# Kernel optimization log

Measured on AMD Instinct MI355X. Metric: run time of the kernel, lower is better.

The kernel has to match this reference:

```python
import jax, jax.numpy as jnp
import numpy as np

CLIP_TANH = 10.0
M_CHECKS, N_VARS = 256, 512   # parity-check matrix shape
ROW_W = 8                     # ones per check row -> E = 256*8 = 2048 edges
BATCH = 16384


def _build_masks():
    """Tanner-graph connectivity masks, as in init_w_skipconn2even / initialize_w_v2c."""
    rng = np.random.default_rng(0)
    pcm = np.zeros((M_CHECKS, N_VARS), np.float32)
    for r in range(M_CHECKS):
        pcm[r, rng.choice(N_VARS, ROW_W, replace=False)] = 1.0
    checks, variables = np.nonzero(pcm)  # edge list, row-major order, length E
    E = checks.size
    # edge e' feeds edge e iff same variable node, different check node
    same_var = variables[:, None] == variables[None, :]
    diff_chk = checks[:, None] != checks[None, :]
    w_odd2even_mask = (same_var & diff_chk).astype(np.float32)               # [E, E]
    # variable v feeds every edge incident to it
    w_skip_mask = (np.arange(N_VARS)[:, None] == variables[None, :]).astype(np.float32)  # [N, E]
    return jnp.asarray(w_odd2even_mask), jnp.asarray(w_skip_mask), E


def setup_inputs() -> dict:
    key = jax.random.key(0)
    w_o2e_mask, w_skip_mask, E = _build_masks()
    k = jax.random.split(key, 5)
    return {
        "x": jax.random.normal(k[0], (BATCH, E), jnp.float32),          # edge messages
        "llr": jax.random.normal(k[1], (BATCH, N_VARS), jnp.float32),   # channel LLRs
        "u": jax.random.uniform(k[2], (E,), jnp.float32),               # dropout uniforms
        "odd_weights": 0.05 * jax.random.normal(k[3], (E, E), jnp.float32),
        "llr_weights": 1.0 + 0.05 * jax.random.normal(k[4], (N_VARS, E), jnp.float32),
        "dropout_logits": 10.0 * jnp.ones((E,), jnp.float32),           # 10000*LOGITS_INIT analogue (sigmoid ~ 1)
        "w_odd2even_mask": w_o2e_mask,
        "w_skipconn2even_mask": w_skip_mask,
    }


def reference(x, llr, u, odd_weights, llr_weights, dropout_logits,
              w_odd2even_mask, w_skipconn2even_mask):
    # TEST-phase forward, mask_only=False
    total_mask = w_odd2even_mask * odd_weights                        # [E, E], very sparse support
    z = (u < jax.nn.sigmoid(dropout_logits)).astype(x.dtype)          # Bernoulli gate per source edge
    mask_after_dropout = total_mask * z[:, None]                      # row-wise gating
    msg = x @ mask_after_dropout                                      # [B, E]
    skip = llr @ (w_skipconn2even_mask * llr_weights)                 # [B, E]
    odd_clamp = jnp.clip(msg + skip, -CLIP_TANH, CLIP_TANH)
    return jnp.tanh(0.5 * odd_clamp)
```

## Files before the change

### kernel.cpp

```cpp
#include <hip/hip_runtime.h>
#include <hip/hip_bf16.h>

constexpr int E     = 2048;
constexpr int NVARS = 512;
constexpr int DMAX  = 20;
constexpr int TB    = 8;
constexpr int NT    = 512;

__device__ __forceinline__ unsigned bf16hi(float f) {
    const unsigned uu = __float_as_uint(f);
    return (uu + 0x7FFFu + ((uu >> 16) & 1u)) & 0xFFFF0000u;
}
__device__ __forceinline__ unsigned pk2(float a, float b) {
    return (bf16hi(a) >> 16) | bf16hi(b);
}
__device__ __forceinline__ float bl(unsigned q) { return __uint_as_float(q << 16); }
__device__ __forceinline__ float bh(unsigned q) { return __uint_as_float(q & 0xFFFF0000u); }

__global__ __launch_bounds__(256)
void k_vsrc(const float* __restrict__ skip_mask,
            const float* __restrict__ llr_w,
            unsigned short* __restrict__ vsrc,
            float* __restrict__ skw)
{
    const int col = blockIdx.x * 256 + threadIdx.x;
    const int v0  = blockIdx.y * (NVARS / 32);
    for (int v = v0; v < v0 + NVARS / 32; ++v) {
        const float m = skip_mask[(size_t)v * E + col];
        if (m != 0.0f) {
            vsrc[col] = (unsigned short)v;
            skw [col] = m * llr_w[(size_t)v * E + col];
        }
    }
}

__global__ __launch_bounds__(64)
void k_pervar(const unsigned short* __restrict__ vsrc,
              const float* __restrict__ skw,
              const float* __restrict__ odd_w,
              const float* __restrict__ u,
              const float* __restrict__ logits,
              unsigned short* __restrict__ mcol,
              unsigned short* __restrict__ wt,
              unsigned int*   __restrict__ itemMeta,
              int*            __restrict__ nitems,
              float2*         __restrict__ meta)
{
    __shared__ unsigned short vs[E];
    __shared__ int deg[NVARS];
    __shared__ unsigned short mem[DMAX];
    __shared__ float zf[DMAX];

    const int v   = blockIdx.x;
    const int tid = threadIdx.x;

    for (int i = tid; i < E / 8; i += 64)
        ((uint4*)vs)[i] = ((const uint4*)vsrc)[i];
    for (int i = tid; i < NVARS; i += 64) deg[i] = 0;
    __syncthreads();
    for (int i = tid; i < E; i += 64) atomicAdd(&deg[vs[i]], 1);
    __syncthreads();

    const int dv = deg[v];

    int itot = 0, vst = 0, ib = 0;
    for (int i = tid; i < NVARS; i += 64) {
        const int d2 = deg[i];
        if (!d2) continue;
        const int dc = (d2 < DMAX) ? d2 : DMAX;
        const int ic = (dc + 3) >> 2;
        itot += ic;
        if (dv > 0 && (d2 < dv || (d2 == dv && i < v))) { vst += d2; ib += ic; }
    }
    #pragma unroll
    for (int o = 32; o; o >>= 1) {
        itot += __shfl_xor(itot, o);
        vst  += __shfl_xor(vst,  o);
        ib   += __shfl_xor(ib,   o);
    }
    if (v == 0 && tid == 0) nitems[0] = itot;
    if (!dv) return;
    const int de = (dv < DMAX) ? dv : DMAX;

    int cnt = 0;
    for (int c = 0; c < E / 64; ++c) {
        const int e = c * 64 + tid;
        const bool m = ((int)vs[e] == v);
        const unsigned long long bal = __ballot(m);
        if (m) {
            const int pos = cnt + __popcll(bal & ((1ull << tid) - 1ull));
            if (pos < DMAX) mem[pos] = (unsigned short)e;
        }
        cnt += __popcll(bal);
    }
    __syncthreads();

    if (tid < de) {
        const int m = mem[tid];
        const float sig = 1.0f / (1.0f + __expf(-logits[m]));
        zf[tid] = (u[m] < sig) ? 1.0f : 0.0f;
        mcol[vst + tid] = (unsigned short)m;
        meta[vst + tid] = make_float2(skw[m], __int_as_float(m | (v << 11)));
    }
    __syncthreads();

    for (int idx = tid; idx < de * de; idx += 64) {
        const int j = idx / de;
        const int i = idx - j * de;
        float ww = 0.0f;
        if (i != j)
            ww = odd_w[(size_t)mem[j] * E + mem[i]] * zf[j];
        wt[(size_t)(vst + j) * DMAX + i] = (unsigned short)(bf16hi(ww) >> 16);
    }

    const int nch = (de + 3) >> 2;
    if (tid < nch)
        itemMeta[ib + tid] = (unsigned)vst | ((unsigned)tid << 11)
                           | ((unsigned)de << 14);
}

__device__ __forceinline__ float th(float s) {
    float c = fminf(fmaxf(s, -10.0f), 10.0f);
    float t = __expf(c);
    return (t - 1.0f) * __frcp_rn(t + 1.0f);
}

__global__ __launch_bounds__(NT, 4)
void fused_main(const float* __restrict__ x,
                const float* __restrict__ llr,
                const unsigned short* __restrict__ mcol,
                const unsigned short* __restrict__ wt,
                const unsigned int*   __restrict__ itemMeta,
                const int*            __restrict__ nitems,
                const float2* __restrict__ meta,
                float* __restrict__ out)
{
    __shared__ uint4 xs[E];
    __shared__ uint4 ls[NVARS];

    const int b0 = blockIdx.x * TB;
    const int t  = threadIdx.x;

    {
        const float4* xr = (const float4*)(x + (size_t)b0 * E);
        const float4 r0 = xr[0 * (E / 4) + t];
        const float4 r1 = xr[1 * (E / 4) + t];
        const float4 r2 = xr[2 * (E / 4) + t];
        const float4 r3 = xr[3 * (E / 4) + t];
        const float4 r4 = xr[4 * (E / 4) + t];
        const float4 r5 = xr[5 * (E / 4) + t];
        const float4 r6 = xr[6 * (E / 4) + t];
        const float4 r7 = xr[7 * (E / 4) + t];
        xs[4 * t + 0] = make_uint4(pk2(r0.x, r1.x), pk2(r2.x, r3.x),
                                   pk2(r4.x, r5.x), pk2(r6.x, r7.x));
        xs[4 * t + 1] = make_uint4(pk2(r0.y, r1.y), pk2(r2.y, r3.y),
                                   pk2(r4.y, r5.y), pk2(r6.y, r7.y));
        xs[4 * t + 2] = make_uint4(pk2(r0.z, r1.z), pk2(r2.z, r3.z),
                                   pk2(r4.z, r5.z), pk2(r6.z, r7.z));
        xs[4 * t + 3] = make_uint4(pk2(r0.w, r1.w), pk2(r2.w, r3.w),
                                   pk2(r4.w, r5.w), pk2(r6.w, r7.w));
    }
    {
        const float* lr = llr + (size_t)b0 * NVARS;
        ls[t] = make_uint4(pk2(lr[t],             lr[NVARS + t]),
                           pk2(lr[2 * NVARS + t], lr[3 * NVARS + t]),
                           pk2(lr[4 * NVARS + t], lr[5 * NVARS + t]),
                           pk2(lr[6 * NVARS + t], lr[7 * NVARS + t]));
    }
    __syncthreads();

    const int nit = nitems[0];

    unsigned sst[2][4][4];
    int      scol[2][4];
    #pragma unroll
    for (int r = 0; r < 2; ++r)
        #pragma unroll
        for (int ii = 0; ii < 4; ++ii) scol[r][ii] = -1;

    #pragma unroll
    for (int r = 0; r < 2; ++r) {
        const int it = r * NT + t;
        if (it < nit) {
            const unsigned im = itemMeta[it];
            const int base = im & 0x7FF;
            const int o0   = ((im >> 11) & 7) << 2;
            const int d    = (im >> 14) & 31;
            int cnt = d - o0; cnt = (cnt < 4) ? cnt : 4;

            const float2 m0 = meta[base];
            const int v = (__float_as_int(m0.y) >> 11) & 0x1FF;
            const uint4 lvq = ls[v];
            const float lf0 = bl(lvq.x), lf1 = bh(lvq.x);
            const float lf2 = bl(lvq.y), lf3 = bh(lvq.y);
            const float lf4 = bl(lvq.z), lf5 = bh(lvq.z);
            const float lf6 = bl(lvq.w), lf7 = bh(lvq.w);

            float a[4][8];
            int cols4[4];
            #pragma unroll
            for (int ii = 0; ii < 4; ++ii) {
                int idx = base + o0 + ii;
                idx = (idx < E) ? idx : (E - 1);
                const float2 mi = meta[idx];
                cols4[ii] = __float_as_int(mi.y) & 0x7FF;
                const float sk = mi.x;
                a[ii][0] = sk * lf0; a[ii][1] = sk * lf1;
                a[ii][2] = sk * lf2; a[ii][3] = sk * lf3;
                a[ii][4] = sk * lf4; a[ii][5] = sk * lf5;
                a[ii][6] = sk * lf6; a[ii][7] = sk * lf7;
            }

            for (int j = 0; j < d; ++j) {
                const int s = mcol[base + j];
                const uint4 xv = xs[s];
                const uint2 wq = *(const uint2*)(wt + (size_t)(base + j) * DMAX + o0);
                const float w0 = bl(wq.x), w1 = bh(wq.x);
                const float w2 = bl(wq.y), w3 = bh(wq.y);
                const float xf0 = bl(xv.x), xf1 = bh(xv.x);
                const float xf2 = bl(xv.y), xf3 = bh(xv.y);
                const float xf4 = bl(xv.z), xf5 = bh(xv.z);
                const float xf6 = bl(xv.w), xf7 = bh(xv.w);
                a[0][0] += w0 * xf0; a[0][1] += w0 * xf1;
                a[0][2] += w0 * xf2; a[0][3] += w0 * xf3;
                a[0][4] += w0 * xf4; a[0][5] += w0 * xf5;
                a[0][6] += w0 * xf6; a[0][7] += w0 * xf7;
                a[1][0] += w1 * xf0; a[1][1] += w1 * xf1;
                a[1][2] += w1 * xf2; a[1][3] += w1 * xf3;
                a[1][4] += w1 * xf4; a[1][5] += w1 * xf5;
                a[1][6] += w1 * xf6; a[1][7] += w1 * xf7;
                a[2][0] += w2 * xf0; a[2][1] += w2 * xf1;
                a[2][2] += w2 * xf2; a[2][3] += w2 * xf3;
                a[2][4] += w2 * xf4; a[2][5] += w2 * xf5;
                a[2][6] += w2 * xf6; a[2][7] += w2 * xf7;
                a[3][0] += w3 * xf0; a[3][1] += w3 * xf1;
                a[3][2] += w3 * xf2; a[3][3] += w3 * xf3;
                a[3][4] += w3 * xf4; a[3][5] += w3 * xf5;
                a[3][6] += w3 * xf6; a[3][7] += w3 * xf7;
            }

            #pragma unroll
            for (int ii = 0; ii < 4; ++ii) {
                if (ii < cnt) {
                    scol[r][ii]   = cols4[ii];
                    sst[r][ii][0] = pk2(th(a[ii][0]), th(a[ii][1]));
                    sst[r][ii][1] = pk2(th(a[ii][2]), th(a[ii][3]));
                    sst[r][ii][2] = pk2(th(a[ii][4]), th(a[ii][5]));
                    sst[r][ii][3] = pk2(th(a[ii][6]), th(a[ii][7]));
                }
            }
        }
    }

    __syncthreads();
    unsigned* osp = (unsigned*)xs;
    #pragma unroll
    for (int r = 0; r < 2; ++r) {
        #pragma unroll
        for (int ii = 0; ii < 4; ++ii) {
            const int c = scol[r][ii];
            if (c >= 0) {
                osp[0 * E + c] = sst[r][ii][0];
                osp[1 * E + c] = sst[r][ii][1];
                osp[2 * E + c] = sst[r][ii][2];
                osp[3 * E + c] = sst[r][ii][3];
            }
        }
    }
    __syncthreads();

    #pragma unroll
    for (int k = 0; k < E / NT; ++k) {
        const int e = k * NT + t;
        #pragma unroll
        for (int p = 0; p < 4; ++p) {
            const unsigned q = osp[p * E + e];
            out[(size_t)(b0 + 2 * p) * E + e]     = bl(q);
            out[(size_t)(b0 + 2 * p + 1) * E + e] = bh(q);
        }
    }
}

extern "C" void kernel_launch(void* const* d_in, const int* in_sizes, int n_in,
                              void* d_out, int out_size, void* d_ws, size_t ws_size,
                              hipStream_t stream) {
    const float* x        = (const float*)d_in[0];
    const float* llr      = (const float*)d_in[1];
    const float* u        = (const float*)d_in[2];
    const float* odd_w    = (const float*)d_in[3];
    const float* llr_w    = (const float*)d_in[4];
    const float* logits   = (const float*)d_in[5];
    const float* skip_msk = (const float*)d_in[7];
    float* out = (float*)d_out;

    const int B = in_sizes[0] / E;

    char* wsb = (char*)d_ws;
    size_t off = 0;
    unsigned short* wt    = (unsigned short*)(wsb + off); off += (size_t)E * DMAX * 2 + 64;
    float2*         meta  = (float2*)(wsb + off);         off += (size_t)E * 8;
    float*          skw   = (float*)(wsb + off);          off += (size_t)E * 4;
    unsigned short* vsrc  = (unsigned short*)(wsb + off); off += (size_t)E * 2;
    unsigned short* mcol  = (unsigned short*)(wsb + off); off += (size_t)E * 2 + 64;
    unsigned int*   itemM = (unsigned int*)(wsb + off);   off += (size_t)1024 * 4;
    int*            nit   = (int*)(wsb + off);            off += 16;

    k_vsrc  <<<dim3(E / 256, 32), dim3(256), 0, stream>>>(skip_msk, llr_w, vsrc, skw);
    k_pervar<<<dim3(NVARS),       dim3(64),  0, stream>>>(vsrc, skw, odd_w, u, logits,
                                                          mcol, wt, itemM, nit, meta);

    fused_main<<<dim3(B / TB), dim3(NT), 0, stream>>>(x, llr, mcol, wt, itemM, nit,
                                                      meta, out);
}
```

Measured before the change: 104.7 us.

## Pack per-item weights and source columns into uint4 records, use hardware bf16 pack

```diff
diff --git a/kernel.cpp b/kernel.cpp
--- a/kernel.cpp
+++ b/kernel.cpp
@@ -11,8 +11,10 @@
     const unsigned uu = __float_as_uint(f);
     return (uu + 0x7FFFu + ((uu >> 16) & 1u)) & 0xFFFF0000u;
 }
-__device__ __forceinline__ unsigned pk2(float a, float b) {
-    return (bf16hi(a) >> 16) | bf16hi(b);
+__device__ __forceinline__ unsigned cvtpk(float lo, float hi) {
+    unsigned r;
+    asm("v_cvt_pk_bf16_f32 %0, %1, %2" : "=v"(r) : "v"(lo), "v"(hi));
+    return r;
 }
 __device__ __forceinline__ float bl(unsigned q) { return __uint_as_float(q << 16); }
 __device__ __forceinline__ float bh(unsigned q) { return __uint_as_float(q & 0xFFFF0000u); }
@@ -40,16 +42,15 @@
               const float* __restrict__ odd_w,
               const float* __restrict__ u,
               const float* __restrict__ logits,
-              unsigned short* __restrict__ mcol,
-              unsigned short* __restrict__ wt,
-              unsigned int*   __restrict__ itemMeta,
-              int*            __restrict__ nitems,
-              float2*         __restrict__ meta)
+              uint4*  __restrict__ wtc,
+              float4* __restrict__ hdr,
+              int*    __restrict__ nitems)
 {
     __shared__ unsigned short vs[E];
     __shared__ int deg[NVARS];
     __shared__ unsigned short mem[DMAX];
     __shared__ float zf[DMAX];
+    __shared__ float sks[DMAX];
 
     const int v   = blockIdx.x;
     const int tid = threadIdx.x;
@@ -63,24 +64,25 @@
 
     const int dv = deg[v];
 
-    int itot = 0, vst = 0, ib = 0;
+    int itot = 0, ib = 0, wb = 0;
     for (int i = tid; i < NVARS; i += 64) {
         const int d2 = deg[i];
         if (!d2) continue;
         const int dc = (d2 < DMAX) ? d2 : DMAX;
         const int ic = (dc + 3) >> 2;
         itot += ic;
-        if (dv > 0 && (d2 < dv || (d2 == dv && i < v))) { vst += d2; ib += ic; }
+        if (dv > 0 && (d2 < dv || (d2 == dv && i < v))) { ib += ic; wb += dc * ic; }
     }
     #pragma unroll
     for (int o = 32; o; o >>= 1) {
         itot += __shfl_xor(itot, o);
-        vst  += __shfl_xor(vst,  o);
         ib   += __shfl_xor(ib,   o);
+        wb   += __shfl_xor(wb,   o);
     }
     if (v == 0 && tid == 0) nitems[0] = itot;
     if (!dv) return;
     const int de = (dv < DMAX) ? dv : DMAX;
+    const int ic = (de + 3) >> 2;
 
     int cnt = 0;
     for (int c = 0; c < E / 64; ++c) {
@@ -98,25 +100,42 @@
     if (tid < de) {
         const int m = mem[tid];
         const float sig = 1.0f / (1.0f + __expf(-logits[m]));
-        zf[tid] = (u[m] < sig) ? 1.0f : 0.0f;
-        mcol[vst + tid] = (unsigned short)m;
-        meta[vst + tid] = make_float2(skw[m], __int_as_float(m | (v << 11)));
-    }
-    __syncthreads();
-
-    for (int idx = tid; idx < de * de; idx += 64) {
-        const int j = idx / de;
-        const int i = idx - j * de;
-        float ww = 0.0f;
-        if (i != j)
-            ww = odd_w[(size_t)mem[j] * E + mem[i]] * zf[j];
-        wt[(size_t)(vst + j) * DMAX + i] = (unsigned short)(bf16hi(ww) >> 16);
-    }
-
-    const int nch = (de + 3) >> 2;
-    if (tid < nch)
-        itemMeta[ib + tid] = (unsigned)vst | ((unsigned)tid << 11)
-                           | ((unsigned)de << 14);
+        zf [tid] = (u[m] < sig) ? 1.0f : 0.0f;
+        sks[tid] = skw[m];
+    }
+    __syncthreads();
+
+    if (tid < ic) {
+        const int o0 = tid * 4;
+        float s0 = 0, s1 = 0, s2 = 0, s3 = 0;
+        unsigned c0 = 0xFFFFu, c1 = 0xFFFFu, c2 = 0xFFFFu, c3 = 0xFFFFu;
+        if (o0 + 0 < de) { s0 = sks[o0 + 0]; c0 = mem[o0 + 0]; }
+        if (o0 + 1 < de) { s1 = sks[o0 + 1]; c1 = mem[o0 + 1]; }
+        if (o0 + 2 < de) { s2 = sks[o0 + 2]; c2 = mem[o0 + 2]; }
+        if (o0 + 3 < de) { s3 = sks[o0 + 3]; c3 = mem[o0 + 3]; }
+        hdr[2 * (ib + tid)]     = make_float4(s0, s1, s2, s3);
+        hdr[2 * (ib + tid) + 1] = make_float4(
+            __uint_as_float(c0 | (c1 << 16)),
+            __uint_as_float(c2 | (c3 << 16)),
+            __uint_as_float((unsigned)(wb + tid * de)),
+            __uint_as_float((unsigned)v | ((unsigned)de << 16)));
+    }
+
+    for (int idx = tid; idx < de * ic; idx += 64) {
+        const int k = idx / de;
+        const int j = idx - k * de;
+        const int src = mem[j];
+        unsigned g[4];
+        #pragma unroll
+        for (int q = 0; q < 4; ++q) {
+            const int o = 4 * k + q;
+            float ww = 0.0f;
+            if (o < de && o != j)
+                ww = odd_w[(size_t)src * E + mem[o]] * zf[j];
+            g[q] = bf16hi(ww) | (unsigned)src;
+        }
+        wtc[wb + idx] = make_uint4(g[0], g[1], g[2], g[3]);
+    }
 }
 
 __device__ __forceinline__ float th(float s) {
@@ -125,14 +144,12 @@
     return (t - 1.0f) * __frcp_rn(t + 1.0f);
 }
 
-__global__ __launch_bounds__(NT, 4)
+__global__ __launch_bounds__(NT, 6)
 void fused_main(const float* __restrict__ x,
                 const float* __restrict__ llr,
-                const unsigned short* __restrict__ mcol,
-                const unsigned short* __restrict__ wt,
-                const unsigned int*   __restrict__ itemMeta,
-                const int*            __restrict__ nitems,
-                const float2* __restrict__ meta,
+                const uint4*  __restrict__ wtc,
+                const float4* __restrict__ hdr,
+                const int*    __restrict__ nitems,
                 float* __restrict__ out)
 {
     __shared__ uint4 xs[E];
@@ -151,45 +168,41 @@
         const float4 r5 = xr[5 * (E / 4) + t];
         const float4 r6 = xr[6 * (E / 4) + t];
         const float4 r7 = xr[7 * (E / 4) + t];
-        xs[4 * t + 0] = make_uint4(pk2(r0.x, r1.x), pk2(r2.x, r3.x),
-                                   pk2(r4.x, r5.x), pk2(r6.x, r7.x));
-        xs[4 * t + 1] = make_uint4(pk2(r0.y, r1.y), pk2(r2.y, r3.y),
-                                   pk2(r4.y, r5.y), pk2(r6.y, r7.y));
-        xs[4 * t + 2] = make_uint4(pk2(r0.z, r1.z), pk2(r2.z, r3.z),
-                                   pk2(r4.z, r5.z), pk2(r6.z, r7.z));
-        xs[4 * t + 3] = make_uint4(pk2(r0.w, r1.w), pk2(r2.w, r3.w),
-                                   pk2(r4.w, r5.w), pk2(r6.w, r7.w));
+        xs[4 * t + 0] = make_uint4(cvtpk(r0.x, r1.x), cvtpk(r2.x, r3.x),
+                                   cvtpk(r4.x, r5.x), cvtpk(r6.x, r7.x));
+        xs[4 * t + 1] = make_uint4(cvtpk(r0.y, r1.y), cvtpk(r2.y, r3.y),
+                                   cvtpk(r4.y, r5.y), cvtpk(r6.y, r7.y));
+        xs[4 * t + 2] = make_uint4(cvtpk(r0.z, r1.z), cvtpk(r2.z, r3.z),
+                                   cvtpk(r4.z, r5.z), cvtpk(r6.z, r7.z));
+        xs[4 * t + 3] = make_uint4(cvtpk(r0.w, r1.w), cvtpk(r2.w, r3.w),
+                                   cvtpk(r4.w, r5.w), cvtpk(r6.w, r7.w));
     }
     {
         const float* lr = llr + (size_t)b0 * NVARS;
-        ls[t] = make_uint4(pk2(lr[t],             lr[NVARS + t]),
-                           pk2(lr[2 * NVARS + t], lr[3 * NVARS + t]),
-                           pk2(lr[4 * NVARS + t], lr[5 * NVARS + t]),
-                           pk2(lr[6 * NVARS + t], lr[7 * NVARS + t]));
+        ls[t] = make_uint4(cvtpk(lr[t],             lr[NVARS + t]),
+                           cvtpk(lr[2 * NVARS + t], lr[3 * NVARS + t]),
+                           cvtpk(lr[4 * NVARS + t], lr[5 * NVARS + t]),
+                           cvtpk(lr[6 * NVARS + t], lr[7 * NVARS + t]));
     }
     __syncthreads();
 
     const int nit = nitems[0];
 
     unsigned sst[2][4][4];
-    int      scol[2][4];
-    #pragma unroll
-    for (int r = 0; r < 2; ++r)
-        #pragma unroll
-        for (int ii = 0; ii < 4; ++ii) scol[r][ii] = -1;
+    unsigned scc[2][2];
 
     #pragma unroll
     for (int r = 0; r < 2; ++r) {
+        scc[r][0] = 0xFFFFFFFFu;
+        scc[r][1] = 0xFFFFFFFFu;
         const int it = r * NT + t;
         if (it < nit) {
-            const unsigned im = itemMeta[it];
-            const int base = im & 0x7FF;
-            const int o0   = ((im >> 11) & 7) << 2;
-            const int d    = (im >> 14) & 31;
-            int cnt = d - o0; cnt = (cnt < 4) ? cnt : 4;
-
-            const float2 m0 = meta[base];
-            const int v = (__float_as_int(m0.y) >> 11) & 0x1FF;
+            const float4 ha = hdr[2 * it];
+            const uint4  hb = ((const uint4*)hdr)[2 * it + 1];
+            const unsigned woff = hb.z;
+            const int v = hb.w & 0xFFFF;
+            const int d = hb.w >> 16;
+
             const uint4 lvq = ls[v];
             const float lf0 = bl(lvq.x), lf1 = bh(lvq.x);
             const float lf2 = bl(lvq.y), lf3 = bh(lvq.y);
@@ -197,26 +210,23 @@
             const float lf6 = bl(lvq.w), lf7 = bh(lvq.w);
 
             float a[4][8];
-            int cols4[4];
             #pragma unroll
             for (int ii = 0; ii < 4; ++ii) {
-                int idx = base + o0 + ii;
-                idx = (idx < E) ? idx : (E - 1);
-                const float2 mi = meta[idx];
-                cols4[ii] = __float_as_int(mi.y) & 0x7FF;
-                const float sk = mi.x;
+                const float sk = (ii == 0) ? ha.x : (ii == 1) ? ha.y
+                               : (ii == 2) ? ha.z : ha.w;
                 a[ii][0] = sk * lf0; a[ii][1] = sk * lf1;
                 a[ii][2] = sk * lf2; a[ii][3] = sk * lf3;
                 a[ii][4] = sk * lf4; a[ii][5] = sk * lf5;
                 a[ii][6] = sk * lf6; a[ii][7] = sk * lf7;
             }
 
+            const uint4* wp = wtc + woff;
             for (int j = 0; j < d; ++j) {
-                const int s = mcol[base + j];
+                const uint4 g = wp[j];
+                const int   s = (int)(g.x & 0x7FFu);
                 const uint4 xv = xs[s];
-                const uint2 wq = *(const uint2*)(wt + (size_t)(base + j) * DMAX + o0);
-                const float w0 = bl(wq.x), w1 = bh(wq.x);
-                const float w2 = bl(wq.y), w3 = bh(wq.y);
+                const float w0 = bh(g.x), w1 = bh(g.y);
+                const float w2 = bh(g.z), w3 = bh(g.w);
                 const float xf0 = bl(xv.x), xf1 = bh(xv.x);
                 const float xf2 = bl(xv.y), xf3 = bh(xv.y);
                 const float xf4 = bl(xv.z), xf5 = bh(xv.z);
@@ -239,15 +249,14 @@
                 a[3][6] += w3 * xf6; a[3][7] += w3 * xf7;
             }
 
+            scc[r][0] = hb.x;
+            scc[r][1] = hb.y;
             #pragma unroll
             for (int ii = 0; ii < 4; ++ii) {
-                if (ii < cnt) {
-                    scol[r][ii]   = cols4[ii];
-                    sst[r][ii][0] = pk2(th(a[ii][0]), th(a[ii][1]));
-                    sst[r][ii][1] = pk2(th(a[ii][2]), th(a[ii][3]));
-                    sst[r][ii][2] = pk2(th(a[ii][4]), th(a[ii][5]));
-                    sst[r][ii][3] = pk2(th(a[ii][6]), th(a[ii][7]));
-                }
+                sst[r][ii][0] = cvtpk(th(a[ii][0]), th(a[ii][1]));
+                sst[r][ii][1] = cvtpk(th(a[ii][2]), th(a[ii][3]));
+                sst[r][ii][2] = cvtpk(th(a[ii][4]), th(a[ii][5]));
+                sst[r][ii][3] = cvtpk(th(a[ii][6]), th(a[ii][7]));
             }
         }
     }
@@ -258,8 +267,8 @@
     for (int r = 0; r < 2; ++r) {
         #pragma unroll
         for (int ii = 0; ii < 4; ++ii) {
-            const int c = scol[r][ii];
-            if (c >= 0) {
+            const unsigned c = (scc[r][ii >> 1] >> ((ii & 1) * 16)) & 0xFFFFu;
+            if (c != 0xFFFFu) {
                 osp[0 * E + c] = sst[r][ii][0];
                 osp[1 * E + c] = sst[r][ii][1];
                 osp[2 * E + c] = sst[r][ii][2];
@@ -297,18 +306,15 @@
 
     char* wsb = (char*)d_ws;
     size_t off = 0;
-    unsigned short* wt    = (unsigned short*)(wsb + off); off += (size_t)E * DMAX * 2 + 64;
-    float2*         meta  = (float2*)(wsb + off);         off += (size_t)E * 8;
-    float*          skw   = (float*)(wsb + off);          off += (size_t)E * 4;
-    unsigned short* vsrc  = (unsigned short*)(wsb + off); off += (size_t)E * 2;
-    unsigned short* mcol  = (unsigned short*)(wsb + off); off += (size_t)E * 2 + 64;
-    unsigned int*   itemM = (unsigned int*)(wsb + off);   off += (size_t)1024 * 4;
-    int*            nit   = (int*)(wsb + off);            off += 16;
+    uint4*          wtc  = (uint4*)(wsb + off);          off += (size_t)6144 * 16;
+    float4*         hdr  = (float4*)(wsb + off);         off += (size_t)1024 * 32;
+    float*          skw  = (float*)(wsb + off);          off += (size_t)E * 4;
+    unsigned short* vsrc = (unsigned short*)(wsb + off); off += (size_t)E * 2;
+    int*            nit  = (int*)(wsb + off);            off += 16;
 
     k_vsrc  <<<dim3(E / 256, 32), dim3(256), 0, stream>>>(skip_msk, llr_w, vsrc, skw);
     k_pervar<<<dim3(NVARS),       dim3(64),  0, stream>>>(vsrc, skw, odd_w, u, logits,
-                                                          mcol, wt, itemM, nit, meta);
-
-    fused_main<<<dim3(B / TB), dim3(NT), 0, stream>>>(x, llr, mcol, wt, itemM, nit,
-                                                      meta, out);
-}
+                                                          wtc, hdr, nit);
+
+    fused_main<<<dim3(B / TB), dim3(NT), 0, stream>>>(x, llr, wtc, hdr, nit, out);
+}
```

Measured after the change: 96.52 us. 1.08x faster.
